# Performance work log

Measured on AMD Instinct MI355X. Metric: run time of the kernel, lower is better.

The kernel has to match this reference:

```python
import jax, jax.numpy as jnp
import numpy as np

PAD_H, PAD_W = 13, 17  # padded grid
GRID_H, GRID_W = 11, 15  # real hex grid (165 hexes)


def _build_convinds() -> np.ndarray:
    """Flat indices into the (13*17,) padded grid of the 7 hex neighbors per cell."""
    off0 = np.array([-17, -16, -1, 0, 1, 17, 18])
    off1 = np.array([-18, -17, -1, 0, 1, 16, 17])
    inds = np.zeros((GRID_H, GRID_W, 7), dtype=np.int32)
    for y in range(1, GRID_H + 1):
        for x in range(1, GRID_W + 1):
            base = y * PAD_W + x
            inds[y - 1, x - 1] = (off0 if y % 2 == 0 else off1) + base
    return inds.reshape(-1)  # (165*7,)


def setup_inputs() -> dict:
    key = jax.random.key(0)
    k1, k2, k3 = jax.random.split(key, 3)
    B, HEXDIM, OUT = 2048, 64, 64
    x = jax.random.normal(k1, (B, 165, HEXDIM), dtype=jnp.float32)
    W = jax.random.normal(k2, (OUT, 7 * HEXDIM), dtype=jnp.float32) * 0.05
    bias = jax.random.normal(k3, (OUT,), dtype=jnp.float32) * 0.05
    return {"x": x, "W": W, "bias": bias}


def reference(x, W, bias):
    convinds = jnp.asarray(_build_convinds())  # static (1155,)
    b, _, hexdim = x.shape
    xg = x.reshape(b, GRID_H, GRID_W, hexdim)
    padded = jnp.zeros((b, PAD_H, PAD_W, hexdim), dtype=x.dtype)
    padded = padded.at[:, 1:GRID_H + 1, 1:GRID_W + 1, :].set(xg)
    padded = padded.reshape(b, PAD_H * PAD_W, hexdim)
    # gather 7 neighbors per hex -> (b, 165, 7*hexdim)
    fc_in = padded[:, convinds, :].reshape(b, 165, 7 * hexdim)
    return jnp.einsum('bnk,ok->bno', fc_in, W) + bias
```

## Files before the change

### kernel.cpp

```cpp
#include <hip/hip_runtime.h>
#include <stdint.h>

typedef __bf16 bf16x8 __attribute__((ext_vector_type(8)));
typedef float floatx4 __attribute__((ext_vector_type(4)));
typedef uint32_t uint32x4 __attribute__((ext_vector_type(4)));

#define GRID_W   15
#define PAD_W    17
#define CELLS    221
#define HEXDIM   64
#define NHEX     165
#define OUTC     64
#define KDIM     448
#define CWORDS   32
#define SXWORDS  (CELLS * CWORDS)

__device__ __forceinline__ uint32_t pack2bf(float a, float b) {
    union { float f; uint32_t u; } ua, ub;
    ua.f = a; ub.f = b;
    uint32_t ra = (ua.u + 0x7fffu + ((ua.u >> 16) & 1u)) >> 16;
    uint32_t rb = (ub.u + 0x7fffu + ((ub.u >> 16) & 1u)) >> 16;
    return ra | (rb << 16);
}

__global__ void wprep_kernel(const float* __restrict__ W, uint32_t* __restrict__ Wbf) {
    int i = blockIdx.x * 256 + threadIdx.x;
    float4 v = ((const float4*)W)[i];
    uint2 p; p.x = pack2bf(v.x, v.y); p.y = pack2bf(v.z, v.w);
    ((uint2*)Wbf)[i] = p;
}

__device__ __forceinline__ floatx4 mfma16(uint32x4 a, uint32x4 b, floatx4 c) {
    return __builtin_amdgcn_mfma_f32_16x16x32_bf16(
        __builtin_bit_cast(bf16x8, a), __builtin_bit_cast(bf16x8, b), c, 0, 0, 0);
}

__global__ __launch_bounds__(512, 4)
void hexconv_kernel(const float* __restrict__ x,
                    const uint32_t* __restrict__ Wbf,
                    const float* __restrict__ bias,
                    float* __restrict__ out)
{
    __shared__ __align__(16) uint32_t sx[SXWORDS];

    const int tid  = threadIdx.x;
    const int b    = blockIdx.x;
    const int wave = tid >> 6;
    const int lane = tid & 63;
    const int col  = lane & 15;
    const int kq   = lane >> 4;
    const int og   = wave & 1;
    const int mg   = wave >> 1;

    const uint32_t* w0 = Wbf + (og * 32 +      col) * (KDIM / 2) + kq * 4;
    const uint32_t* w1 = Wbf + (og * 32 + 16 + col) * (KDIM / 2) + kq * 4;

    uint32x4 wf[2][7];
    #pragma unroll
    for (int ksl = 0; ksl < 7; ++ksl) {
        wf[0][ksl] = *(const uint32x4*)(w0 + ksl * 16);
        wf[1][ksl] = *(const uint32x4*)(w1 + ksl * 16);
    }

    {
        const float4* xs = (const float4*)(x + (size_t)b * NHEX * HEXDIM);
        for (int i = tid; i < NHEX * HEXDIM / 4; i += 512) {
            int n = i >> 4;
            int d = i & 15;
            float4 v = xs[i];
            int y0 = n / GRID_W, x0 = n - y0 * GRID_W;
            int cell = (y0 + 1) * PAD_W + (x0 + 1);
            int pc   = (d >> 1) ^ (cell & 7);
            uint32_t* dst = sx + cell * CWORDS + pc * 4 + (d & 1) * 2;
            uint2 p; p.x = pack2bf(v.x, v.y); p.y = pack2bf(v.z, v.w);
            *(uint2*)dst = p;
        }
        for (int i = tid; i < 56 * 8; i += 512) {
            int c = i >> 3, ch = i & 7;
            int cell;
            if (c < 17)      cell = c;
            else if (c < 34) cell = 12 * PAD_W + (c - 17);
            else if (c < 45) cell = (c - 33) * PAD_W;
            else             cell = (c - 44) * PAD_W + 16;
            uint32x4 z = {0u, 0u, 0u, 0u};
            *(uint32x4*)(sx + cell * CWORDS + ch * 4) = z;
        }
    }
    __syncthreads();

    const int off0[7] = {-17, -16, -1, 0, 1, 17, 18};
    const int off1[7] = {-18, -17, -1, 0, 1, 16, 17};

    floatx4 acc[3][2];
    #pragma unroll
    for (int m = 0; m < 3; ++m) {
        acc[m][0] = (floatx4){0.f, 0.f, 0.f, 0.f};
        acc[m][1] = (floatx4){0.f, 0.f, 0.f, 0.f};
    }

    #pragma unroll
    for (int half = 0; half < 2; ++half) {
        if (half == 1) {
            #pragma unroll
            for (int ksl = 0; ksl < 7; ++ksl) {
                wf[0][ksl] = *(const uint32x4*)(w0 + 112 + ksl * 16);
                wf[1][ksl] = *(const uint32x4*)(w1 + 112 + ksl * 16);
            }
        }
        #pragma unroll
        for (int mt3 = 0; mt3 < 3; ++mt3) {
            const int mt = mg * 3 + mt3;
            int n = mt * 16 + col;
            bool valid = (n < NHEX);
            int nn = valid ? n : 0;
            int y0 = nn / GRID_W, x0 = nn - y0 * GRID_W;
            int base = (y0 + 1) * PAD_W + (x0 + 1);
            bool use0 = (y0 & 1);
            #pragma unroll
            for (int ksl = 0; ksl < 7; ++ksl) {
                const int ks = half * 7 + ksl;
                const int j  = ks >> 1;
                const int h  = ks & 1;
                int c  = valid ? (base + (use0 ? off0[j] : off1[j])) : 16;
                int ch = ((h * 4 + kq) ^ (c & 7));
                uint32x4 bv = *(const uint32x4*)(sx + c * CWORDS + ch * 4);
                acc[mt3][0] = mfma16(wf[0][ksl], bv, acc[mt3][0]);
                acc[mt3][1] = mfma16(wf[1][ksl], bv, acc[mt3][1]);
            }
        }
    }

    float4 b40 = *(const float4*)(bias + og * 32 + kq * 4);
    float4 b41 = *(const float4*)(bias + og * 32 + 16 + kq * 4);
    float* outb = out + (size_t)b * NHEX * OUTC;
    #pragma unroll
    for (int mt3 = 0; mt3 < 3; ++mt3) {
        int n = (mg * 3 + mt3) * 16 + col;
        if (n < NHEX) {
            float* po = outb + (size_t)n * OUTC + og * 32 + kq * 4;
            float4 v0, v1;
            v0.x = acc[mt3][0][0] + b40.x; v0.y = acc[mt3][0][1] + b40.y;
            v0.z = acc[mt3][0][2] + b40.z; v0.w = acc[mt3][0][3] + b40.w;
            v1.x = acc[mt3][1][0] + b41.x; v1.y = acc[mt3][1][1] + b41.y;
            v1.z = acc[mt3][1][2] + b41.z; v1.w = acc[mt3][1][3] + b41.w;
            *(float4*)po        = v0;
            *(float4*)(po + 16) = v1;
        }
    }
}

extern "C" void kernel_launch(void* const* d_in, const int* in_sizes, int n_in,
                              void* d_out, int out_size, void* d_ws, size_t ws_size,
                              hipStream_t stream) {
    const float* x    = (const float*)d_in[0];
    const float* W    = (const float*)d_in[1];
    const float* bias = (const float*)d_in[2];
    float* out        = (float*)d_out;
    uint32_t* Wbf     = (uint32_t*)d_ws;

    wprep_kernel<<<28, 256, 0, stream>>>(W, Wbf);

    int B = in_sizes[0] / (NHEX * HEXDIM);
    hexconv_kernel<<<B, 512, 0, stream>>>(x, Wbf, bias, out);
}
```

Baseline: 197.5 us.

## Process four samples per block with double-buffered LDS prefetch of next sample

Each block now handles four batch samples instead of one. While the current sample's MFMA work runs, the next sample's input is loaded from global memory into registers, then converted and written into a second LDS buffer. The scatter offsets are precomputed once and the border-zeroing is done once for both buffers. The aim is to hide global load latency and amortize block setup, at the cost of fewer blocks (512), double the LDS, and more register pressure from the prefetched values.

```diff
diff --git a/kernel.cpp b/kernel.cpp
--- a/kernel.cpp
+++ b/kernel.cpp
@@ -14,6 +14,8 @@
 #define KDIM     448
 #define CWORDS   32
 #define SXWORDS  (CELLS * CWORDS)
+#define SPB      4
+#define XF4      (NHEX * HEXDIM / 4)
 
 __device__ __forceinline__ uint32_t pack2bf(float a, float b) {
     union { float f; uint32_t u; } ua, ub;
@@ -39,12 +41,11 @@
 void hexconv_kernel(const float* __restrict__ x,
                     const uint32_t* __restrict__ Wbf,
                     const float* __restrict__ bias,
-                    float* __restrict__ out)
+                    float* __restrict__ out, int B)
 {
-    __shared__ __align__(16) uint32_t sx[SXWORDS];
+    __shared__ __align__(16) uint32_t sx[2 * SXWORDS];
 
     const int tid  = threadIdx.x;
-    const int b    = blockIdx.x;
     const int wave = tid >> 6;
     const int lane = tid & 63;
     const int col  = lane & 15;
@@ -52,38 +53,50 @@
     const int og   = wave & 1;
     const int mg   = wave >> 1;
 
-    const uint32_t* w0 = Wbf + (og * 32 +      col) * (KDIM / 2) + kq * 4;
-    const uint32_t* w1 = Wbf + (og * 32 + 16 + col) * (KDIM / 2) + kq * 4;
-
-    uint32x4 wf[2][7];
+    const uint32_t* w0 = Wbf + (og * 32 + col) * (KDIM / 2) + kq * 4;
+    const uint32_t* w1 = w0 + 16 * (KDIM / 2);
+
+    int dstoff[6];
     #pragma unroll
-    for (int ksl = 0; ksl < 7; ++ksl) {
-        wf[0][ksl] = *(const uint32x4*)(w0 + ksl * 16);
-        wf[1][ksl] = *(const uint32x4*)(w1 + ksl * 16);
-    }
-
-    {
-        const float4* xs = (const float4*)(x + (size_t)b * NHEX * HEXDIM);
-        for (int i = tid; i < NHEX * HEXDIM / 4; i += 512) {
-            int n = i >> 4;
-            int d = i & 15;
-            float4 v = xs[i];
-            int y0 = n / GRID_W, x0 = n - y0 * GRID_W;
-            int cell = (y0 + 1) * PAD_W + (x0 + 1);
-            int pc   = (d >> 1) ^ (cell & 7);
-            uint32_t* dst = sx + cell * CWORDS + pc * 4 + (d & 1) * 2;
-            uint2 p; p.x = pack2bf(v.x, v.y); p.y = pack2bf(v.z, v.w);
-            *(uint2*)dst = p;
-        }
-        for (int i = tid; i < 56 * 8; i += 512) {
-            int c = i >> 3, ch = i & 7;
-            int cell;
-            if (c < 17)      cell = c;
-            else if (c < 34) cell = 12 * PAD_W + (c - 17);
-            else if (c < 45) cell = (c - 33) * PAD_W;
-            else             cell = (c - 44) * PAD_W + 16;
-            uint32x4 z = {0u, 0u, 0u, 0u};
-            *(uint32x4*)(sx + cell * CWORDS + ch * 4) = z;
+    for (int j = 0; j < 6; ++j) {
+        int i  = tid + j * 512;
+        int ii = (i < XF4) ? i : 0;
+        int n = ii >> 4, d = ii & 15;
+        int y0 = n / GRID_W, x0 = n - y0 * GRID_W;
+        int cell = (y0 + 1) * PAD_W + (x0 + 1);
+        int pc   = (d >> 1) ^ (cell & 7);
+        dstoff[j] = cell * CWORDS + pc * 4 + (d & 1) * 2;
+    }
+
+    const int s0 = blockIdx.x * SPB;
+    const float4* xs0 = (const float4*)x + (size_t)s0 * XF4;
+
+    float4 pv[6];
+    if (s0 < B) {
+        #pragma unroll
+        for (int j = 0; j < 5; ++j) pv[j] = xs0[tid + j * 512];
+        if (tid < XF4 - 5 * 512) pv[5] = xs0[tid + 5 * 512];
+    }
+    if (tid < 56 * 8) {
+        int c = tid >> 3, ch = tid & 7;
+        int cell;
+        if (c < 17)      cell = c;
+        else if (c < 34) cell = 12 * PAD_W + (c - 17);
+        else if (c < 45) cell = (c - 33) * PAD_W;
+        else             cell = (c - 44) * PAD_W + 16;
+        uint32x4 z = {0u, 0u, 0u, 0u};
+        *(uint32x4*)(sx + cell * CWORDS + ch * 4) = z;
+        *(uint32x4*)(sx + SXWORDS + cell * CWORDS + ch * 4) = z;
+    }
+    if (s0 < B) {
+        #pragma unroll
+        for (int j = 0; j < 5; ++j) {
+            uint2 p; p.x = pack2bf(pv[j].x, pv[j].y); p.y = pack2bf(pv[j].z, pv[j].w);
+            *(uint2*)(sx + dstoff[j]) = p;
+        }
+        if (tid < XF4 - 5 * 512) {
+            uint2 p; p.x = pack2bf(pv[5].x, pv[5].y); p.y = pack2bf(pv[5].z, pv[5].w);
+            *(uint2*)(sx + dstoff[5]) = p;
         }
     }
     __syncthreads();
@@ -91,60 +104,103 @@
     const int off0[7] = {-17, -16, -1, 0, 1, 17, 18};
     const int off1[7] = {-18, -17, -1, 0, 1, 16, 17};
 
-    floatx4 acc[3][2];
     #pragma unroll
-    for (int m = 0; m < 3; ++m) {
-        acc[m][0] = (floatx4){0.f, 0.f, 0.f, 0.f};
-        acc[m][1] = (floatx4){0.f, 0.f, 0.f, 0.f};
-    }
-
-    #pragma unroll
-    for (int half = 0; half < 2; ++half) {
-        if (half == 1) {
-            #pragma unroll
-            for (int ksl = 0; ksl < 7; ++ksl) {
-                wf[0][ksl] = *(const uint32x4*)(w0 + 112 + ksl * 16);
-                wf[1][ksl] = *(const uint32x4*)(w1 + 112 + ksl * 16);
-            }
-        }
-        #pragma unroll
-        for (int mt3 = 0; mt3 < 3; ++mt3) {
-            const int mt = mg * 3 + mt3;
-            int n = mt * 16 + col;
-            bool valid = (n < NHEX);
-            int nn = valid ? n : 0;
-            int y0 = nn / GRID_W, x0 = nn - y0 * GRID_W;
-            int base = (y0 + 1) * PAD_W + (x0 + 1);
-            bool use0 = (y0 & 1);
-            #pragma unroll
-            for (int ksl = 0; ksl < 7; ++ksl) {
-                const int ks = half * 7 + ksl;
-                const int j  = ks >> 1;
-                const int h  = ks & 1;
-                int c  = valid ? (base + (use0 ? off0[j] : off1[j])) : 16;
-                int ch = ((h * 4 + kq) ^ (c & 7));
-                uint32x4 bv = *(const uint32x4*)(sx + c * CWORDS + ch * 4);
-                acc[mt3][0] = mfma16(wf[0][ksl], bv, acc[mt3][0]);
-                acc[mt3][1] = mfma16(wf[1][ksl], bv, acc[mt3][1]);
-            }
-        }
-    }
-
-    float4 b40 = *(const float4*)(bias + og * 32 + kq * 4);
-    float4 b41 = *(const float4*)(bias + og * 32 + 16 + kq * 4);
-    float* outb = out + (size_t)b * NHEX * OUTC;
-    #pragma unroll
-    for (int mt3 = 0; mt3 < 3; ++mt3) {
-        int n = (mg * 3 + mt3) * 16 + col;
-        if (n < NHEX) {
-            float* po = outb + (size_t)n * OUTC + og * 32 + kq * 4;
-            float4 v0, v1;
-            v0.x = acc[mt3][0][0] + b40.x; v0.y = acc[mt3][0][1] + b40.y;
-            v0.z = acc[mt3][0][2] + b40.z; v0.w = acc[mt3][0][3] + b40.w;
-            v1.x = acc[mt3][1][0] + b41.x; v1.y = acc[mt3][1][1] + b41.y;
-            v1.z = acc[mt3][1][2] + b41.z; v1.w = acc[mt3][1][3] + b41.w;
-            *(float4*)po        = v0;
-            *(float4*)(po + 16) = v1;
+    for (int s = 0; s < SPB; ++s) {
+        const bool sval = (s0 + s) < B;
+        const bool nval = (s + 1 < SPB) && ((s0 + s + 1) < B);
+
+        float4 sv[6];
+        if (nval) {
+            const float4* xsn = xs0 + (size_t)(s + 1) * XF4;
+            #pragma unroll
+            for (int j = 0; j < 5; ++j) sv[j] = xsn[tid + j * 512];
+            if (tid < XF4 - 5 * 512) sv[5] = xsn[tid + 5 * 512];
+        }
+
+        if (sval) {
+            const uint32_t* sb = sx + (s & 1) * SXWORDS;
+
+            int base3[3]; int use3[3]; int valid3[3];
+            #pragma unroll
+            for (int mt3 = 0; mt3 < 3; ++mt3) {
+                int mt = mg * 3 + mt3;
+                int n  = mt * 16 + col;
+                bool valid = (n < NHEX);
+                int nn = valid ? n : 0;
+                int y0 = nn / GRID_W, x0 = nn - y0 * GRID_W;
+                base3[mt3]  = (y0 + 1) * PAD_W + (x0 + 1);
+                use3[mt3]   = (y0 & 1);
+                valid3[mt3] = valid;
+            }
+
+            floatx4 acc[3][2];
+            #pragma unroll
+            for (int m = 0; m < 3; ++m) {
+                acc[m][0] = (floatx4){0.f, 0.f, 0.f, 0.f};
+                acc[m][1] = (floatx4){0.f, 0.f, 0.f, 0.f};
+            }
+
+            #pragma unroll
+            for (int half = 0; half < 2; ++half) {
+                uint32x4 wf[2][7];
+                #pragma unroll
+                for (int ksl = 0; ksl < 7; ++ksl) {
+                    wf[0][ksl] = *(const uint32x4*)(w0 + half * 112 + ksl * 16);
+                    wf[1][ksl] = *(const uint32x4*)(w1 + half * 112 + ksl * 16);
+                }
+                #pragma unroll
+                for (int mt3 = 0; mt3 < 3; ++mt3) {
+                    const int mt = mg * 3 + mt3;
+                    if (mt * 16 < NHEX) {
+                        #pragma unroll
+                        for (int ksl = 0; ksl < 7; ++ksl) {
+                            const int ks = half * 7 + ksl;
+                            const int j  = ks >> 1;
+                            const int h  = ks & 1;
+                            int c  = valid3[mt3] ? (base3[mt3] + (use3[mt3] ? off0[j] : off1[j]))
+                                                 : 16;
+                            int ch = ((h * 4 + kq) ^ (c & 7));
+                            uint32x4 bv = *(const uint32x4*)(sb + c * CWORDS + ch * 4);
+                            acc[mt3][0] = mfma16(wf[0][ksl], bv, acc[mt3][0]);
+                            acc[mt3][1] = mfma16(wf[1][ksl], bv, acc[mt3][1]);
+                        }
+                    }
+                }
+            }
+
+            float4 b40 = *(const float4*)(bias + og * 32 + kq * 4);
+            float4 b41 = *(const float4*)(bias + og * 32 + 16 + kq * 4);
+            float* outb = out + (size_t)(s0 + s) * NHEX * OUTC;
+            #pragma unroll
+            for (int mt3 = 0; mt3 < 3; ++mt3) {
+                int n = (mg * 3 + mt3) * 16 + col;
+                if (n < NHEX) {
+                    float* po = outb + (size_t)n * OUTC + og * 32 + kq * 4;
+                    float4 v0, v1;
+                    v0.x = acc[mt3][0][0] + b40.x; v0.y = acc[mt3][0][1] + b40.y;
+                    v0.z = acc[mt3][0][2] + b40.z; v0.w = acc[mt3][0][3] + b40.w;
+                    v1.x = acc[mt3][1][0] + b41.x; v1.y = acc[mt3][1][1] + b41.y;
+                    v1.z = acc[mt3][1][2] + b41.z; v1.w = acc[mt3][1][3] + b41.w;
+                    *(float4*)po        = v0;
+                    *(float4*)(po + 16) = v1;
+                }
+            }
+        }
+
+        if (s + 1 < SPB) {
+            if (nval) {
+                uint32_t* db = sx + ((s + 1) & 1) * SXWORDS;
+                #pragma unroll
+                for (int j = 0; j < 5; ++j) {
+                    uint2 p; p.x = pack2bf(sv[j].x, sv[j].y); p.y = pack2bf(sv[j].z, sv[j].w);
+                    *(uint2*)(db + dstoff[j]) = p;
+                }
+                if (tid < XF4 - 5 * 512) {
+                    uint2 p; p.x = pack2bf(sv[5].x, sv[5].y); p.y = pack2bf(sv[5].z, sv[5].w);
+                    *(uint2*)(db + dstoff[5]) = p;
+                }
+            }
+            __syncthreads();
         }
     }
 }
@@ -161,5 +217,6 @@
     wprep_kernel<<<28, 256, 0, stream>>>(W, Wbf);
 
     int B = in_sizes[0] / (NHEX * HEXDIM);
-    hexconv_kernel<<<B, 512, 0, stream>>>(x, Wbf, bias, out);
-}
+    int nb = (B + SPB - 1) / SPB;
+    hexconv_kernel<<<nb, 512, 0, stream>>>(x, Wbf, bias, out, B);
+}
```

After: 359.7 us. 82.1% more time.

## Give each wave private LDS row band and split channel halves across two passes

Applied to the files above, without the earlier changes.

Each block now has 4 waves instead of 8. Each wave owns a private 6-row band of the padded grid in LDS and loads the input half-channel by half-channel. Block-wide __syncthreads is replaced by per-wave lgkmcnt waits. Each wave now computes all 64 output channels with 4 accumulators per M-tile, and reads weight fragments straight from global or cache inside the loop rather than holding them in registers. The weight-prep layout is reordered so each half-K slice is contiguous. This trades block-level sync and a shared full tile for duplicated halo loads, and relies on per-wave fences being enough for correctness.

```diff
diff --git a/kernel.cpp b/kernel.cpp
--- a/kernel.cpp
+++ b/kernel.cpp
@@ -7,13 +7,13 @@
 
 #define GRID_W   15
 #define PAD_W    17
-#define CELLS    221
+#define NHEX     165
 #define HEXDIM   64
-#define NHEX     165
 #define OUTC     64
 #define KDIM     448
-#define CWORDS   32
-#define SXWORDS  (CELLS * CWORDS)
+#define CS       20
+#define BROWS    6
+#define BWORDS   (BROWS * PAD_W * CS)
 
 __device__ __forceinline__ uint32_t pack2bf(float a, float b) {
     union { float f; uint32_t u; } ua, ub;
@@ -23,11 +23,21 @@
     return ra | (rb << 16);
 }
 
+__device__ __forceinline__ void lds_fence() {
+    __builtin_amdgcn_sched_barrier(0);
+    asm volatile("s_waitcnt lgkmcnt(0)" ::: "memory");
+    __builtin_amdgcn_sched_barrier(0);
+}
+
 __global__ void wprep_kernel(const float* __restrict__ W, uint32_t* __restrict__ Wbf) {
-    int i = blockIdx.x * 256 + threadIdx.x;
-    float4 v = ((const float4*)W)[i];
-    uint2 p; p.x = pack2bf(v.x, v.y); p.y = pack2bf(v.z, v.w);
-    ((uint2*)Wbf)[i] = p;
+    int o = blockIdx.x;
+    int r = threadIdx.x;
+    if (r < 224) {
+        int H = r / 112, rr = r - H * 112;
+        int j = rr >> 4, w = rr & 15;
+        const float* src = W + o * KDIM + j * 64 + H * 32 + w * 2;
+        Wbf[o * 224 + r] = pack2bf(src[0], src[1]);
+    }
 }
 
 __device__ __forceinline__ floatx4 mfma16(uint32x4 a, uint32x4 b, floatx4 c) {
@@ -35,116 +45,120 @@
         __builtin_bit_cast(bf16x8, a), __builtin_bit_cast(bf16x8, b), c, 0, 0, 0);
 }
 
-__global__ __launch_bounds__(512, 4)
+__global__ __launch_bounds__(256, 4)
 void hexconv_kernel(const float* __restrict__ x,
                     const uint32_t* __restrict__ Wbf,
                     const float* __restrict__ bias,
-                    float* __restrict__ out)
+                    float* __restrict__ out, int B)
 {
-    __shared__ __align__(16) uint32_t sx[SXWORDS];
+    __shared__ __align__(16) uint32_t sx[4 * BWORDS];
 
     const int tid  = threadIdx.x;
-    const int b    = blockIdx.x;
-    const int wave = tid >> 6;
+    const int mg   = tid >> 6;
     const int lane = tid & 63;
     const int col  = lane & 15;
     const int kq   = lane >> 4;
-    const int og   = wave & 1;
-    const int mg   = wave >> 1;
+    const int s    = blockIdx.x;
 
-    const uint32_t* w0 = Wbf + (og * 32 +      col) * (KDIM / 2) + kq * 4;
-    const uint32_t* w1 = Wbf + (og * 32 + 16 + col) * (KDIM / 2) + kq * 4;
+    uint32_t* wb = sx + mg * BWORDS;
+    const int prow0 = mg * 3;
 
-    uint32x4 wf[2][7];
     #pragma unroll
-    for (int ksl = 0; ksl < 7; ++ksl) {
-        wf[0][ksl] = *(const uint32x4*)(w0 + ksl * 16);
-        wf[1][ksl] = *(const uint32x4*)(w1 + ksl * 16);
-    }
-
-    {
-        const float4* xs = (const float4*)(x + (size_t)b * NHEX * HEXDIM);
-        for (int i = tid; i < NHEX * HEXDIM / 4; i += 512) {
-            int n = i >> 4;
-            int d = i & 15;
-            float4 v = xs[i];
-            int y0 = n / GRID_W, x0 = n - y0 * GRID_W;
-            int cell = (y0 + 1) * PAD_W + (x0 + 1);
-            int pc   = (d >> 1) ^ (cell & 7);
-            uint32_t* dst = sx + cell * CWORDS + pc * 4 + (d & 1) * 2;
-            uint2 p; p.x = pack2bf(v.x, v.y); p.y = pack2bf(v.z, v.w);
-            *(uint2*)dst = p;
-        }
-        for (int i = tid; i < 56 * 8; i += 512) {
-            int c = i >> 3, ch = i & 7;
-            int cell;
-            if (c < 17)      cell = c;
-            else if (c < 34) cell = 12 * PAD_W + (c - 17);
-            else if (c < 45) cell = (c - 33) * PAD_W;
-            else             cell = (c - 44) * PAD_W + 16;
+    for (int it = 0; it < 8; ++it) {
+        int i = lane + it * 64;
+        if (i < BWORDS / 4) {
             uint32x4 z = {0u, 0u, 0u, 0u};
-            *(uint32x4*)(sx + cell * CWORDS + ch * 4) = z;
+            *(uint32x4*)(wb + i * 4) = z;
         }
     }
-    __syncthreads();
+    lds_fence();
 
     const int off0[7] = {-17, -16, -1, 0, 1, 17, 18};
     const int off1[7] = {-18, -17, -1, 0, 1, 16, 17};
-
-    floatx4 acc[3][2];
+    int base3[3], use3[3];
     #pragma unroll
-    for (int m = 0; m < 3; ++m) {
-        acc[m][0] = (floatx4){0.f, 0.f, 0.f, 0.f};
-        acc[m][1] = (floatx4){0.f, 0.f, 0.f, 0.f};
+    for (int mt3 = 0; mt3 < 3; ++mt3) {
+        int n = (mg * 3 + mt3) * 16 + col;
+        bool valid = (n < NHEX);
+        int nn = valid ? n : 0;
+        int y0 = nn / GRID_W, x0 = nn - y0 * GRID_W;
+        int bl = (y0 + 1 - prow0) * PAD_W + (x0 + 1);
+        base3[mt3] = valid ? bl : 34;
+        use3[mt3]  = (y0 & 1);
     }
 
+    const float4* xs = (const float4*)(x + (size_t)s * NHEX * HEXDIM);
+
+    floatx4 acc[3][4];
     #pragma unroll
-    for (int half = 0; half < 2; ++half) {
-        if (half == 1) {
-            #pragma unroll
-            for (int ksl = 0; ksl < 7; ++ksl) {
-                wf[0][ksl] = *(const uint32x4*)(w0 + 112 + ksl * 16);
-                wf[1][ksl] = *(const uint32x4*)(w1 + 112 + ksl * 16);
+    for (int m = 0; m < 3; ++m)
+        #pragma unroll
+        for (int ot = 0; ot < 4; ++ot)
+            acc[m][ot] = (floatx4){0.f, 0.f, 0.f, 0.f};
+
+    const uint32_t* wq = Wbf + col * 224 + kq * 4;
+
+    #pragma unroll
+    for (int H = 0; H < 2; ++H) {
+        #pragma unroll
+        for (int r = 0; r < BROWS; ++r) {
+            int y0 = prow0 + r - 1;
+            if (y0 >= 0 && y0 <= 10) {
+                #pragma unroll
+                for (int it = 0; it < 2; ++it) {
+                    int i = lane + it * 64;
+                    if (i < 120) {
+                        int nr = i >> 3, d = i & 7;
+                        float4 v = xs[(y0 * GRID_W + nr) * 16 + H * 8 + d];
+                        uint2 p;
+                        p.x = pack2bf(v.x, v.y); p.y = pack2bf(v.z, v.w);
+                        *(uint2*)(wb + (r * PAD_W + nr + 1) * CS + d * 2) = p;
+                    }
+                }
             }
         }
+        lds_fence();
+
         #pragma unroll
-        for (int mt3 = 0; mt3 < 3; ++mt3) {
-            const int mt = mg * 3 + mt3;
-            int n = mt * 16 + col;
-            bool valid = (n < NHEX);
-            int nn = valid ? n : 0;
-            int y0 = nn / GRID_W, x0 = nn - y0 * GRID_W;
-            int base = (y0 + 1) * PAD_W + (x0 + 1);
-            bool use0 = (y0 & 1);
+        for (int j = 0; j < 7; ++j) {
+            uint32x4 wf0 = *(const uint32x4*)(wq +      0 + H * 112 + j * 16);
+            uint32x4 wf1 = *(const uint32x4*)(wq +   3584 + H * 112 + j * 16);
+            uint32x4 wf2 = *(const uint32x4*)(wq +   7168 + H * 112 + j * 16);
+            uint32x4 wf3 = *(const uint32x4*)(wq +  10752 + H * 112 + j * 16);
             #pragma unroll
-            for (int ksl = 0; ksl < 7; ++ksl) {
-                const int ks = half * 7 + ksl;
-                const int j  = ks >> 1;
-                const int h  = ks & 1;
-                int c  = valid ? (base + (use0 ? off0[j] : off1[j])) : 16;
-                int ch = ((h * 4 + kq) ^ (c & 7));
-                uint32x4 bv = *(const uint32x4*)(sx + c * CWORDS + ch * 4);
-                acc[mt3][0] = mfma16(wf[0][ksl], bv, acc[mt3][0]);
-                acc[mt3][1] = mfma16(wf[1][ksl], bv, acc[mt3][1]);
+            for (int mt3 = 0; mt3 < 3; ++mt3) {
+                if ((mg * 3 + mt3) * 16 < NHEX) {
+                    int c = base3[mt3] + (use3[mt3] ? off0[j] : off1[j]);
+                    uint32x4 bv = *(const uint32x4*)(wb + c * CS + kq * 4);
+                    acc[mt3][0] = mfma16(wf0, bv, acc[mt3][0]);
+                    acc[mt3][1] = mfma16(wf1, bv, acc[mt3][1]);
+                    acc[mt3][2] = mfma16(wf2, bv, acc[mt3][2]);
+                    acc[mt3][3] = mfma16(wf3, bv, acc[mt3][3]);
+                }
             }
         }
+        lds_fence();
     }
 
-    float4 b40 = *(const float4*)(bias + og * 32 + kq * 4);
-    float4 b41 = *(const float4*)(bias + og * 32 + 16 + kq * 4);
-    float* outb = out + (size_t)b * NHEX * OUTC;
+    float* outb = out + (size_t)s * NHEX * OUTC;
+    float4 b4[4];
+    #pragma unroll
+    for (int ot = 0; ot < 4; ++ot)
+        b4[ot] = *(const float4*)(bias + ot * 16 + kq * 4);
     #pragma unroll
     for (int mt3 = 0; mt3 < 3; ++mt3) {
         int n = (mg * 3 + mt3) * 16 + col;
         if (n < NHEX) {
-            float* po = outb + (size_t)n * OUTC + og * 32 + kq * 4;
-            float4 v0, v1;
-            v0.x = acc[mt3][0][0] + b40.x; v0.y = acc[mt3][0][1] + b40.y;
-            v0.z = acc[mt3][0][2] + b40.z; v0.w = acc[mt3][0][3] + b40.w;
-            v1.x = acc[mt3][1][0] + b41.x; v1.y = acc[mt3][1][1] + b41.y;
-            v1.z = acc[mt3][1][2] + b41.z; v1.w = acc[mt3][1][3] + b41.w;
-            *(float4*)po        = v0;
-            *(float4*)(po + 16) = v1;
+            float* po = outb + (size_t)n * OUTC + kq * 4;
+            #pragma unroll
+            for (int ot = 0; ot < 4; ++ot) {
+                float4 o4;
+                o4.x = acc[mt3][ot][0] + b4[ot].x;
+                o4.y = acc[mt3][ot][1] + b4[ot].y;
+                o4.z = acc[mt3][ot][2] + b4[ot].z;
+                o4.w = acc[mt3][ot][3] + b4[ot].w;
+                *(float4*)(po + ot * 16) = o4;
+            }
         }
     }
 }
@@ -158,8 +172,8 @@
     float* out        = (float*)d_out;
     uint32_t* Wbf     = (uint32_t*)d_ws;
 
-    wprep_kernel<<<28, 256, 0, stream>>>(W, Wbf);
+    wprep_kernel<<<64, 256, 0, stream>>>(W, Wbf);
 
     int B = in_sizes[0] / (NHEX * HEXDIM);
-    hexconv_kernel<<<B, 512, 0, stream>>>(x, Wbf, bias, out);
+    hexconv_kernel<<<B, 256, 0, stream>>>(x, Wbf, bias, out, B);
 }
```

Result: slower. 202.4 us (+2.5%).
